# Optimization experiments

Hardware: AMD Instinct MI355X
Metric: run time of the kernel (lower is better)

Reference implementation:

```python
import jax, jax.numpy as jnp
import numpy as np

N_PATHOLOGY = 14      # NUM_PATHOLOGY_NODES (CheXpert/NIH pathology count)
NEG_SLOPE = 0.2       # PyG GATv2Conv default negative_slope


def gatv2_layer(x, src, dst, n_nodes, Wl, bl, Wr, br, att, bias, concat):
    """PyG GATv2Conv (share_weights=False, dropout inactive in eval).
    Wl/bl: source (lin_l) transform; Wr/br: target (lin_r) transform.
    att: [H, C] attention vector; bias: output bias.
    """
    H, C = att.shape
    xl = (x @ Wl + bl).reshape(-1, H, C)   # [N, H, C] source features
    xr = (x @ Wr + br).reshape(-1, H, C)   # [N, H, C] target features
    xj = xl[src]                            # [E, H, C] gathered source msgs
    xi = xr[dst]                            # [E, H, C] gathered targets
    s = jax.nn.leaky_relu(xi + xj, NEG_SLOPE)
    e = jnp.einsum('ehc,hc->eh', s, att)    # [E, H] raw attention logits
    # segment softmax over incoming edges of each destination node
    m = jax.ops.segment_max(e, dst, num_segments=n_nodes)      # [N, H]
    e = jnp.exp(e - m[dst])
    denom = jax.ops.segment_sum(e, dst, num_segments=n_nodes)  # [N, H]
    alpha = e / (denom[dst] + 1e-16)
    out = jax.ops.segment_sum(alpha[:, :, None] * xj, dst, num_segments=n_nodes)
    out = out.reshape(n_nodes, H * C) if concat else out.mean(axis=1)
    return out + bias


def setup_inputs() -> dict:
    key = jax.random.key(0)
    ks = jax.random.split(key, 16)
    N, E, D, H = 10000, 50000, 768, 4
    s = 0.02
    inp = {
        'x': jax.random.normal(ks[0], (N, D), jnp.float32),
        'edge_index': jax.random.randint(ks[1], (2, E), 0, N, jnp.int32),
        # layer 1: in=768 -> heads=4, out=768 (concat -> 3072)
        'Wl1': jax.random.normal(ks[2], (D, H * D), jnp.float32) * s,
        'bl1': jnp.zeros((H * D,), jnp.float32),
        'Wr1': jax.random.normal(ks[3], (D, H * D), jnp.float32) * s,
        'br1': jnp.zeros((H * D,), jnp.float32),
        'att1': jax.random.normal(ks[4], (H, D), jnp.float32) * s,
        'bias1': jnp.zeros((H * D,), jnp.float32),
        # layer 2: in=3072 -> heads=1, out=768 (mean/no-concat)
        'Wl2': jax.random.normal(ks[5], (H * D, D), jnp.float32) * s,
        'bl2': jnp.zeros((D,), jnp.float32),
        'Wr2': jax.random.normal(ks[6], (H * D, D), jnp.float32) * s,
        'br2': jnp.zeros((D,), jnp.float32),
        'att2': jax.random.normal(ks[7], (1, D), jnp.float32) * s,
        'bias2': jnp.zeros((D,), jnp.float32),
    }
    return inp


def reference(x, edge_index, Wl1, bl1, Wr1, br1, att1, bias1,
              Wl2, bl2, Wr2, br2, att2, bias2):
    n = x.shape[0]
    # PyG GATv2Conv adds self loops by default
    loops = jnp.arange(n, dtype=edge_index.dtype)
    src = jnp.concatenate([edge_index[0], loops])
    dst = jnp.concatenate([edge_index[1], loops])
    h = gatv2_layer(x, src, dst, n, Wl1, bl1, Wr1, br1, att1, bias1, True)
    h = jax.nn.relu(h)  # dropout is identity in eval mode
    out = gatv2_layer(h, src, dst, n, Wl2, bl2, Wr2, br2, att2, bias2, False)
    return out[:N_PATHOLOGY]
```

## Files before the change

kernel.cpp:

```cpp
#include <hip/hip_runtime.h>
#include <cstdint>
#include <cstddef>

#define N_PATH 14
#define NEG_SLOPE 0.2f
#define BINW 128
#define NZ2 4

using u16 = unsigned short;
using u32 = unsigned int;
typedef __attribute__((ext_vector_type(4))) float f32x4;
typedef __attribute__((ext_vector_type(8))) short bf16x8;

__device__ __forceinline__ float lrelu(float v) { return v > 0.f ? v : NEG_SLOPE * v; }
__device__ __forceinline__ u16 f2bf(float f) {
    union { float f; u32 u; } c; c.f = f;
    return (u16)((c.u + 0x7FFFu + ((c.u >> 16) & 1u)) >> 16);
}
__device__ __forceinline__ float bf2f(u16 v) {
    union { u32 u; float f; } c; c.u = ((u32)v) << 16; return c.f;
}

__global__ void k_init(int* __restrict__ mapBC, int nMap,
                       u32* __restrict__ z, int nZ)
{
    int stride = gridDim.x * blockDim.x;
    int i0 = blockIdx.x * blockDim.x + threadIdx.x;
    for (int i = i0; i < nMap; i += stride) mapBC[i] = -1;
    for (int i = i0; i < nZ; i += stride) z[i] = 0;
}

__global__ void k_build2(const int* __restrict__ esrc, const int* __restrict__ edst,
                         int E, int Nn,
                         int* __restrict__ mapB, int* __restrict__ listB,
                         int* __restrict__ cnt,
                         int* __restrict__ deg2, int* __restrict__ e2bin,
                         int capB)
{
    int e = blockIdx.x * blockDim.x + threadIdx.x;
    int ET = E + Nn;
    if (e >= ET) return;
    int s, d;
    if (e < E) { s = esrc[e]; d = edst[e]; } else { s = e - E; d = s; }
    if (d >= N_PATH) return;
    int slot = atomicAdd(&deg2[d], 1);
    if (slot < BINW) e2bin[d * BINW + slot] = s;
    int old = atomicCAS(&mapB[s], -1, -2);
    if (old == -1) {
        int idx = atomicAdd(&cnt[0], 1);
        if (idx < capB) listB[idx] = s;
        mapB[s] = idx;
    }
}

__global__ void k_build1(const int* __restrict__ esrc, const int* __restrict__ edst,
                         int E, int Nn,
                         const int* __restrict__ mapB,
                         int* __restrict__ mapC, int* __restrict__ listC,
                         int* __restrict__ cnt,
                         int* __restrict__ deg1, int* __restrict__ e1bin,
                         int capB, int capC)
{
    int e = blockIdx.x * blockDim.x + threadIdx.x;
    int ET = E + Nn;
    if (e >= ET) return;
    int s, d;
    if (e < E) { s = esrc[e]; d = edst[e]; } else { s = e - E; d = s; }
    int b = mapB[d];
    if (b < 0 || b >= capB) return;
    int slot = atomicAdd(&deg1[b], 1);
    if (slot < BINW) e1bin[b * BINW + slot] = s;
    int old = atomicCAS(&mapC[s], -1, -2);
    if (old == -1) {
        int idx = atomicAdd(&cnt[1], 1);
        if (idx < capC) listC[idx] = s;
        mapC[s] = idx;
    }
}

__global__ void k_gatherA(const float* __restrict__ x,
                          const int* __restrict__ listC, const int* __restrict__ listB,
                          const int* __restrict__ mapC, const int* __restrict__ cnt,
                          u16* __restrict__ Abf, int* __restrict__ listBinC,
                          int capB, int capC)
{
    int bid = blockIdx.x;
    int t = threadIdx.x;
    if (bid == capC) {
        int nB = cnt[0]; if (nB > capB) nB = capB;
        for (int i = t; i < capB; i += 192) {
            int v = 0;
            if (i < nB) {
                v = mapC[listB[i]];
                if (v < 0) v = 0;
                if (v >= capC) v = capC - 1;
            }
            listBinC[i] = v;
        }
        return;
    }
    int nC = cnt[1]; if (nC > capC) nC = capC;
    if (bid >= nC) return;
    int g = listC[bid];
    float4 v = *reinterpret_cast<const float4*>(x + (size_t)g * 768 + t * 4);
    uint2 o;
    o.x = (u32)f2bf(v.x) | ((u32)f2bf(v.y) << 16);
    o.y = (u32)f2bf(v.z) | ((u32)f2bf(v.w) << 16);
    *reinterpret_cast<uint2*>(Abf + (size_t)bid * 768 + t * 4) = o;
}

__device__ __forceinline__
void gemm_tile(const u16* __restrict__ A, int lda,
               const int* __restrict__ gather,
               const float* __restrict__ W, int ldw, int nColOff,
               const float* __restrict__ bias,
               void* __restrict__ Cout, int ldc, int mode,
               int M, int bx, int by, int k0, int kchunk,
               u16* __restrict__ As, u16* __restrict__ Bs)
{
    int m0 = by * 64;
    if (m0 >= M) return;
    int n0 = bx * 64;
    int t = threadIdx.x;
    int lane = t & 63, wave = t >> 6;
    int wr = wave >> 1, wc = wave & 1;
    int lrow = lane & 15, lhi = lane >> 4;

    int chunk = t & 7;
    int rowp[2], aRow[2], wIdx[2];
    #pragma unroll
    for (int p = 0; p < 2; ++p) {
        rowp[p] = p * 32 + (t >> 3);
        int ar = m0 + rowp[p]; if (ar >= M) ar = M - 1;
        aRow[p] = gather ? gather[ar] : ar;
        wIdx[p] = rowp[p] * 64 + ((chunk ^ (rowp[p] & 7)) << 3);
    }
    int bk = t >> 4;
    int bn = (t & 15) << 2;

    int aIdx[2][2], bIdx[2][2];
    #pragma unroll
    for (int mi = 0; mi < 2; ++mi)
        #pragma unroll
        for (int ks = 0; ks < 2; ++ks) {
            int ra = wr * 32 + mi * 16 + lrow;
            aIdx[mi][ks] = ra * 64 + ((((ks << 2) | lhi) ^ (ra & 7)) << 3);
            int rb = wc * 32 + mi * 16 + lrow;
            bIdx[mi][ks] = rb * 64 + ((((ks << 2) | lhi) ^ (rb & 7)) << 3);
        }

    f32x4 acc[2][2];
    #pragma unroll
    for (int i = 0; i < 2; ++i)
        #pragma unroll
        for (int j = 0; j < 2; ++j)
            acc[i][j] = (f32x4){0.f, 0.f, 0.f, 0.f};

    for (int kt = 0; kt < kchunk; kt += 64) {
        int kb = k0 + kt;
        #pragma unroll
        for (int p = 0; p < 2; ++p) {
            uint4 av = *reinterpret_cast<const uint4*>(
                A + (size_t)aRow[p] * lda + kb + chunk * 8);
            *reinterpret_cast<uint4*>(&As[wIdx[p]]) = av;
        }
        #pragma unroll
        for (int p = 0; p < 4; ++p) {
            int kk = p * 16 + bk;
            const float* wp = W + (size_t)(kb + kk) * ldw + nColOff + n0 + bn;
            float4 wv = *reinterpret_cast<const float4*>(wp);
            float wa[4] = {wv.x, wv.y, wv.z, wv.w};
            #pragma unroll
            for (int j = 0; j < 4; ++j) {
                int n = bn + j;
                int pc = (kk & 7) | ((((kk >> 3) & 7) ^ (n & 7)) << 3);
                Bs[n * 64 + pc] = f2bf(wa[j]);
            }
        }
        __syncthreads();
        #pragma unroll
        for (int ks = 0; ks < 2; ++ks) {
            bf16x8 a0 = *reinterpret_cast<const bf16x8*>(&As[aIdx[0][ks]]);
            bf16x8 a1 = *reinterpret_cast<const bf16x8*>(&As[aIdx[1][ks]]);
            bf16x8 b0 = *reinterpret_cast<const bf16x8*>(&Bs[bIdx[0][ks]]);
            bf16x8 b1 = *reinterpret_cast<const bf16x8*>(&Bs[bIdx[1][ks]]);
            acc[0][0] = __builtin_amdgcn_mfma_f32_16x16x32_bf16(a0, b0, acc[0][0], 0, 0, 0);
            acc[0][1] = __builtin_amdgcn_mfma_f32_16x16x32_bf16(a0, b1, acc[0][1], 0, 0, 0);
            acc[1][0] = __builtin_amdgcn_mfma_f32_16x16x32_bf16(a1, b0, acc[1][0], 0, 0, 0);
            acc[1][1] = __builtin_amdgcn_mfma_f32_16x16x32_bf16(a1, b1, acc[1][1], 0, 0, 0);
        }
        __syncthreads();
    }

    #pragma unroll
    for (int mi = 0; mi < 2; ++mi)
        #pragma unroll
        for (int ni = 0; ni < 2; ++ni) {
            int gc = n0 + wc * 32 + ni * 16 + lrow;
            float bv = (mode == 2) ? bias[gc] : 0.f;
            #pragma unroll
            for (int j = 0; j < 4; ++j) {
                int gr = m0 + wr * 32 + mi * 16 + lhi * 4 + j;
                if (gr < M) {
                    float v = acc[mi][ni][j] + bv;
                    if (mode == 2) ((u16*)Cout)[(size_t)gr * ldc + gc] = f2bf(v);
                    else           ((float*)Cout)[(size_t)gr * ldc + gc] = v;
                }
            }
        }
}

__global__ __launch_bounds__(256)
void k_gemm1(const u16* __restrict__ Abf, const int* __restrict__ listBinC,
             const float* __restrict__ Wl1, const float* __restrict__ Wr1,
             const float* __restrict__ bl1, const float* __restrict__ br1,
             u16* __restrict__ XL1, u16* __restrict__ XR1,
             const int* __restrict__ cnt, int capC, int capB)
{
    __shared__ __align__(16) u16 As[64 * 64];
    __shared__ __align__(16) u16 Bs[64 * 64];
    int partA = 48 * (capC / 64);
    int bid = blockIdx.x;
    if (bid < partA) {
        int nC = cnt[1]; if (nC > capC) nC = capC;
        gemm_tile(Abf, 768, nullptr, Wl1, 3072, 0, bl1, XL1, 3072, 2,
                  nC, bid % 48, bid / 48, 0, 768, As, Bs);
    } else {
        bid -= partA;
        int nB = cnt[0]; if (nB > capB) nB = capB;
        gemm_tile(Abf, 768, listBinC, Wr1, 3072, 0, br1, XR1, 3072, 2,
                  nB, bid % 48, bid / 48, 0, 768, As, Bs);
    }
}

__global__ __launch_bounds__(256)
void k_gemm2(const u16* __restrict__ H1bf,
             const float* __restrict__ Wl2, const float* __restrict__ Wr2,
             float* __restrict__ XLR2,
             const int* __restrict__ cnt, int capB)
{
    __shared__ __align__(16) u16 As[64 * 64];
    __shared__ __align__(16) u16 Bs[64 * 64];
    int nB = cnt[0]; if (nB > capB) nB = capB;
    int z = blockIdx.z;
    int n0 = blockIdx.x * 64;
    bool hi = n0 >= 768;
    const float* W = hi ? Wr2 : Wl2;
    int nColOff = hi ? -768 : 0;
    const int kchunk = 3072 / NZ2;
    float* Cp = XLR2 + (size_t)z * capB * 1536;
    gemm_tile(H1bf, 3072, nullptr, W, 768, nColOff, nullptr, Cp, 1536, 0,
              nB, blockIdx.x, blockIdx.y, z * kchunk, kchunk, As, Bs);
}

__global__ __launch_bounds__(256)
void k_fused1(const u16* __restrict__ XL1, const u16* __restrict__ XR1,
              const float* __restrict__ att1, const float* __restrict__ bias1,
              const int* __restrict__ mapC,
              const int* __restrict__ deg1, const int* __restrict__ e1bin,
              u16* __restrict__ H1bf,
              const int* __restrict__ cnt, int capB, int capC)
{
    __shared__ int sIdx[BINW];
    int b = blockIdx.x;
    int nB = cnt[0]; if (nB > capB) nB = capB;
    if (b >= nB) return;
    int t = threadIdx.x;
    int n = deg1[b]; if (n > BINW) n = BINW;
    if (t < n) {
        int c = mapC[e1bin[b * BINW + t]];
        if (c < 0) c = 0; if (c >= capC) c = capC - 1;
        sIdx[t] = c;
    }
    __syncthreads();

    int base = t * 12;
    float xr[12], av[12];
    {
        const u16* p = XR1 + (size_t)b * 3072 + base;
        uint2 q0 = *reinterpret_cast<const uint2*>(p);
        uint2 q1 = *reinterpret_cast<const uint2*>(p + 4);
        uint2 q2 = *reinterpret_cast<const uint2*>(p + 8);
        u32 w[6] = {q0.x, q0.y, q1.x, q1.y, q2.x, q2.y};
        #pragma unroll
        for (int j = 0; j < 6; ++j) {
            xr[2*j]   = bf2f((u16)(w[j] & 0xFFFF));
            xr[2*j+1] = bf2f((u16)(w[j] >> 16));
        }
        float4 a0 = *reinterpret_cast<const float4*>(att1 + base);
        float4 a1 = *reinterpret_cast<const float4*>(att1 + base + 4);
        float4 a2 = *reinterpret_cast<const float4*>(att1 + base + 8);
        av[0]=a0.x; av[1]=a0.y; av[2]=a0.z; av[3]=a0.w;
        av[4]=a1.x; av[5]=a1.y; av[6]=a1.z; av[7]=a1.w;
        av[8]=a2.x; av[9]=a2.y; av[10]=a2.z; av[11]=a2.w;
    }

    float acc[12];
    #pragma unroll
    for (int j = 0; j < 12; ++j) acc[j] = 0.f;
    float sumex = 0.f;

    uint2 q0, q1, q2;
    if (n > 0) {
        const u16* p = XL1 + (size_t)sIdx[0] * 3072 + base;
        q0 = *reinterpret_cast<const uint2*>(p);
        q1 = *reinterpret_cast<const uint2*>(p + 4);
        q2 = *reinterpret_cast<const uint2*>(p + 8);
    }
    for (int i = 0; i < n; ++i) {
        uint2 r0 = q0, r1 = q1, r2 = q2;
        if (i + 1 < n) {
            const u16* p = XL1 + (size_t)sIdx[i + 1] * 3072 + base;
            q0 = *reinterpret_cast<const uint2*>(p);
            q1 = *reinterpret_cast<const uint2*>(p + 4);
            q2 = *reinterpret_cast<const uint2*>(p + 8);
        }
        float xl[12];
        u32 w[6] = {r0.x, r0.y, r1.x, r1.y, r2.x, r2.y};
        #pragma unroll
        for (int j = 0; j < 6; ++j) {
            xl[2*j]   = bf2f((u16)(w[j] & 0xFFFF));
            xl[2*j+1] = bf2f((u16)(w[j] >> 16));
        }
        float pa = 0.f;
        #pragma unroll
        for (int j = 0; j < 12; ++j)
            pa = fmaf(av[j], lrelu(xl[j] + xr[j]), pa);
        #pragma unroll
        for (int off = 32; off > 0; off >>= 1) pa += __shfl_xor(pa, off);
        float ex = expf(pa);
        sumex += ex;
        #pragma unroll
        for (int j = 0; j < 12; ++j) acc[j] = fmaf(ex, xl[j], acc[j]);
    }

    float inv = 1.f / (sumex + 1e-16f);
    u32 o[6];
    #pragma unroll
    for (int j = 0; j < 6; ++j) {
        float v0 = acc[2*j]   * inv + bias1[base + 2*j];
        float v1 = acc[2*j+1] * inv + bias1[base + 2*j+1];
        v0 = v0 > 0.f ? v0 : 0.f;
        v1 = v1 > 0.f ? v1 : 0.f;
        o[j] = (u32)f2bf(v0) | ((u32)f2bf(v1) << 16);
    }
    u16* q = H1bf + (size_t)b * 3072 + base;
    uint2 s0; s0.x = o[0]; s0.y = o[1];
    uint2 s1; s1.x = o[2]; s1.y = o[3];
    uint2 s2; s2.x = o[4]; s2.y = o[5];
    *reinterpret_cast<uint2*>(q)     = s0;
    *reinterpret_cast<uint2*>(q + 4) = s1;
    *reinterpret_cast<uint2*>(q + 8) = s2;
}

__global__ __launch_bounds__(256)
void k_fused2(const float* __restrict__ XLR2,
              const float* __restrict__ att2, const float* __restrict__ bias2,
              const float* __restrict__ bl2, const float* __restrict__ br2,
              const int* __restrict__ mapB,
              const int* __restrict__ deg2, const int* __restrict__ e2bin,
              float* __restrict__ out, int capB)
{
    __shared__ int sIdx[BINW];
    __shared__ float sAcc[4][768];
    __shared__ float sSum[4];
    const size_t PART = (size_t)capB * 1536;
    int a = blockIdx.x;
    int t = threadIdx.x;
    int wv = t >> 6, lane = t & 63;
    int n = deg2[a]; if (n > BINW) n = BINW;
    if (t < n) {
        int bs = mapB[e2bin[a * BINW + t]];
        if (bs < 0) bs = 0; if (bs >= capB) bs = capB - 1;
        sIdx[t] = bs;
    }
    __syncthreads();

    int base = lane * 12;
    int bd = mapB[a];
    if (bd < 0) bd = 0; if (bd >= capB) bd = capB - 1;

    float xr[12], av[12], blv[12];
    {
        const float* p = XLR2 + (size_t)bd * 1536 + 768 + base;
        #pragma unroll
        for (int j = 0; j < 12; ++j) xr[j] = br2[base + j];
        for (int z = 0; z < NZ2; ++z)
            #pragma unroll
            for (int j = 0; j < 12; ++j) xr[j] += p[z * PART + j];
        #pragma unroll
        for (int j = 0; j < 12; ++j) { av[j] = att2[base + j]; blv[j] = bl2[base + j]; }
    }

    float acc[12];
    #pragma unroll
    for (int j = 0; j < 12; ++j) acc[j] = 0.f;
    float sumex = 0.f;

    for (int i = wv; i < n; i += 4) {
        int bs = sIdx[i];
        const float* p = XLR2 + (size_t)bs * 1536 + base;
        float xl[12];
        #pragma unroll
        for (int j = 0; j < 12; ++j) xl[j] = blv[j];
        for (int z = 0; z < NZ2; ++z)
            #pragma unroll
            for (int j = 0; j < 12; ++j) xl[j] += p[z * PART + j];
        float pa = 0.f;
        #pragma unroll
        for (int j = 0; j < 12; ++j)
            pa = fmaf(av[j], lrelu(xl[j] + xr[j]), pa);
        #pragma unroll
        for (int off = 32; off > 0; off >>= 1) pa += __shfl_xor(pa, off);
        float ex = expf(pa);
        sumex += ex;
        #pragma unroll
        for (int j = 0; j < 12; ++j) acc[j] = fmaf(ex, xl[j], acc[j]);
    }

    if (lane == 0) sSum[wv] = sumex;
    #pragma unroll
    for (int j = 0; j < 12; ++j) sAcc[wv][base + j] = acc[j];
    __syncthreads();

    float tot = sSum[0] + sSum[1] + sSum[2] + sSum[3];
    float inv = 1.f / (tot + 1e-16f);
    for (int c = t; c < 768; c += 256) {
        float s = sAcc[0][c] + sAcc[1][c] + sAcc[2][c] + sAcc[3][c];
        out[(size_t)a * 768 + c] = s * inv + bias2[c];
    }
}

struct Lay {
    size_t mapB, mapC;
    size_t zbase, zbytes;
    size_t cnt, deg2, deg1;
    size_t listB, listC, listBinC, e1bin, e2bin;
    size_t Abf, XL1, XR1, H1bf, XLR2;
    size_t total;
};

static Lay makeLayout(int Nn, int cB, int cC)
{
    Lay L{};
    size_t off = 0;
    auto take = [&](size_t bytes) { size_t o = (off + 255) & ~(size_t)255; off = o + bytes; return o; };
    L.mapB = take((size_t)2 * Nn * 4);
    L.mapC = L.mapB + (size_t)Nn * 4;
    size_t zo = 0;
    size_t cntO  = zo; zo += 64;
    size_t deg2O = zo; zo += 64 * 4;
    size_t deg1O = zo; zo += (size_t)cB * 4;
    L.zbase = take(zo); L.zbytes = zo;
    L.cnt  = L.zbase + cntO;
    L.deg2 = L.zbase + deg2O;
    L.deg1 = L.zbase + deg1O;
    L.listB    = take((size_t)cB * 4);
    L.listC    = take((size_t)cC * 4);
    L.listBinC = take((size_t)cB * 4);
    L.e1bin = take((size_t)cB * BINW * 4);
    L.e2bin = take((size_t)16 * BINW * 4);
    L.Abf  = take((size_t)cC * 768 * 2);
    L.XL1  = take((size_t)cC * 3072 * 2);
    L.XR1  = take((size_t)cB * 3072 * 2);
    L.H1bf = take((size_t)cB * 3072 * 2);
    L.XLR2 = take((size_t)NZ2 * cB * 1536 * 4);
    L.total = off;
    return L;
}

extern "C" void kernel_launch(void* const* d_in, const int* in_sizes, int n_in,
                              void* d_out, int out_size, void* d_ws, size_t ws_size,
                              hipStream_t stream)
{
    const float* x     = (const float*)d_in[0];
    const int*   ei    = (const int*)  d_in[1];
    const float* Wl1   = (const float*)d_in[2];
    const float* bl1   = (const float*)d_in[3];
    const float* Wr1   = (const float*)d_in[4];
    const float* br1   = (const float*)d_in[5];
    const float* att1  = (const float*)d_in[6];
    const float* bias1 = (const float*)d_in[7];
    const float* Wl2   = (const float*)d_in[8];
    const float* bl2   = (const float*)d_in[9];
    const float* Wr2   = (const float*)d_in[10];
    const float* br2   = (const float*)d_in[11];
    const float* att2  = (const float*)d_in[12];
    const float* bias2 = (const float*)d_in[13];
    float* out = (float*)d_out;

    int Nn = in_sizes[0] / 768;
    int E  = in_sizes[1] / 2;
    const int* esrc = ei;
    const int* edst = ei + E;
    int ET = E + Nn;

    static const int tiers[2][2] = { {256, 1024}, {128, 768} };
    int capB = tiers[1][0], capC = tiers[1][1];
    Lay L = makeLayout(Nn, capB, capC);
    for (int t = 0; t < 2; ++t) {
        Lay cand = makeLayout(Nn, tiers[t][0], tiers[t][1]);
        if (cand.total <= ws_size) { capB = tiers[t][0]; capC = tiers[t][1]; L = cand; break; }
    }

    char* ws = (char*)d_ws;
    int*   mapB     = (int*)  (ws + L.mapB);
    int*   mapC     = (int*)  (ws + L.mapC);
    int*   cnt      = (int*)  (ws + L.cnt);
    int*   deg2     = (int*)  (ws + L.deg2);
    int*   deg1     = (int*)  (ws + L.deg1);
    int*   listB    = (int*)  (ws + L.listB);
    int*   listC    = (int*)  (ws + L.listC);
    int*   listBinC = (int*)  (ws + L.listBinC);
    int*   e1bin    = (int*)  (ws + L.e1bin);
    int*   e2bin    = (int*)  (ws + L.e2bin);
    u16*   Abf      = (u16*)  (ws + L.Abf);
    u16*   XL1      = (u16*)  (ws + L.XL1);
    u16*   XR1      = (u16*)  (ws + L.XR1);
    u16*   H1bf     = (u16*)  (ws + L.H1bf);
    float* XLR2     = (float*)(ws + L.XLR2);

    k_init<<<256, 256, 0, stream>>>((int*)(ws + L.mapB), 2 * Nn,
                                    (u32*)(ws + L.zbase), (int)(L.zbytes / 4));

    int bgrid = (ET + 255) / 256;
    k_build2<<<bgrid, 256, 0, stream>>>(esrc, edst, E, Nn, mapB, listB, cnt,
                                        deg2, e2bin, capB);
    k_build1<<<bgrid, 256, 0, stream>>>(esrc, edst, E, Nn, mapB, mapC, listC, cnt,
                                        deg1, e1bin, capB, capC);

    k_gatherA<<<capC + 1, 192, 0, stream>>>(x, listC, listB, mapC, cnt,
                                            Abf, listBinC, capB, capC);

    int g1 = 48 * (capC / 64) + 48 * (capB / 64);
    k_gemm1<<<g1, 256, 0, stream>>>(Abf, listBinC, Wl1, Wr1, bl1, br1,
                                    XL1, XR1, cnt, capC, capB);

    k_fused1<<<capB, 256, 0, stream>>>(XL1, XR1, att1, bias1, mapC, deg1, e1bin,
                                       H1bf, cnt, capB, capC);

    k_gemm2<<<dim3(24, capB / 64, NZ2), 256, 0, stream>>>(H1bf, Wl2, Wr2, XLR2,
                                                          cnt, capB);

    k_fused2<<<N_PATH, 256, 0, stream>>>(XLR2, att2, bias2, bl2, br2, mapB,
                                         deg2, e2bin, out, capB);
}
```

Measured before the change: 87.54 us.

## Fuse all stages into one persistent kernel with software grid barriers

Replaces the seven separate launches (two graph builds, gather, two GEMMs, two fused attention stages) with one persistent 512-block kernel. The stages are separated by an atomic-counter grid barrier, and the kernel sizes its GEMM tile loops from the actual node counts. The aim is to remove per-launch overhead and the tail gaps between small kernels. In exchange it relies on all 512 blocks being co-resident (otherwise the barrier deadlocks), adds barrier latency, and puts the small stages on idle or oversubscribed blocks.

```diff
diff --git a/kernel.cpp b/kernel.cpp
--- a/kernel.cpp
+++ b/kernel.cpp
@@ -6,6 +6,7 @@
 #define NEG_SLOPE 0.2f
 #define BINW 128
 #define NZ2 4
+#define NBLK 512
 
 using u16 = unsigned short;
 using u32 = unsigned int;
@@ -20,6 +21,42 @@
 __device__ __forceinline__ float bf2f(u16 v) {
     union { u32 u; float f; } c; c.u = ((u32)v) << 16; return c.f;
 }
+__device__ __forceinline__ int imin(int a, int b) { return a < b ? a : b; }
+
+struct Params {
+    const float* x; const int* esrc; const int* edst;
+    const float *Wl1, *bl1, *Wr1, *br1, *att1, *bias1;
+    const float *Wl2, *bl2, *Wr2, *br2, *att2, *bias2;
+    float* out;
+    int *mapB, *mapC, *cnt; unsigned* bar; int *deg2, *deg1;
+    int *listB, *listC, *listBinC, *e1bin, *e2bin;
+    u16 *Abf, *XL1, *XR1, *H1bf; float* XLR2;
+    int Nn, E, capB, capC;
+};
+
+__device__ __forceinline__ void gridbar(unsigned* bar, unsigned& mygen)
+{
+    __syncthreads();
+    if (threadIdx.x == 0) {
+        __threadfence();
+        unsigned nblk = gridDim.x;
+        unsigned prev = atomicAdd(&bar[0], 1u);
+        if (prev == nblk - 1u) {
+            atomicExch(&bar[0], 0u);
+            __threadfence();
+            atomicAdd(&bar[1], 1u);
+        } else {
+            unsigned g;
+            do {
+                __builtin_amdgcn_s_sleep(4);
+                g = __hip_atomic_load(&bar[1], __ATOMIC_RELAXED, __HIP_MEMORY_SCOPE_AGENT);
+            } while (g == mygen);
+        }
+        mygen++;
+        __threadfence();
+    }
+    __syncthreads();
+}
 
 __global__ void k_init(int* __restrict__ mapBC, int nMap,
                        u32* __restrict__ z, int nZ)
@@ -28,85 +65,6 @@
     int i0 = blockIdx.x * blockDim.x + threadIdx.x;
     for (int i = i0; i < nMap; i += stride) mapBC[i] = -1;
     for (int i = i0; i < nZ; i += stride) z[i] = 0;
-}
-
-__global__ void k_build2(const int* __restrict__ esrc, const int* __restrict__ edst,
-                         int E, int Nn,
-                         int* __restrict__ mapB, int* __restrict__ listB,
-                         int* __restrict__ cnt,
-                         int* __restrict__ deg2, int* __restrict__ e2bin,
-                         int capB)
-{
-    int e = blockIdx.x * blockDim.x + threadIdx.x;
-    int ET = E + Nn;
-    if (e >= ET) return;
-    int s, d;
-    if (e < E) { s = esrc[e]; d = edst[e]; } else { s = e - E; d = s; }
-    if (d >= N_PATH) return;
-    int slot = atomicAdd(&deg2[d], 1);
-    if (slot < BINW) e2bin[d * BINW + slot] = s;
-    int old = atomicCAS(&mapB[s], -1, -2);
-    if (old == -1) {
-        int idx = atomicAdd(&cnt[0], 1);
-        if (idx < capB) listB[idx] = s;
-        mapB[s] = idx;
-    }
-}
-
-__global__ void k_build1(const int* __restrict__ esrc, const int* __restrict__ edst,
-                         int E, int Nn,
-                         const int* __restrict__ mapB,
-                         int* __restrict__ mapC, int* __restrict__ listC,
-                         int* __restrict__ cnt,
-                         int* __restrict__ deg1, int* __restrict__ e1bin,
-                         int capB, int capC)
-{
-    int e = blockIdx.x * blockDim.x + threadIdx.x;
-    int ET = E + Nn;
-    if (e >= ET) return;
-    int s, d;
-    if (e < E) { s = esrc[e]; d = edst[e]; } else { s = e - E; d = s; }
-    int b = mapB[d];
-    if (b < 0 || b >= capB) return;
-    int slot = atomicAdd(&deg1[b], 1);
-    if (slot < BINW) e1bin[b * BINW + slot] = s;
-    int old = atomicCAS(&mapC[s], -1, -2);
-    if (old == -1) {
-        int idx = atomicAdd(&cnt[1], 1);
-        if (idx < capC) listC[idx] = s;
-        mapC[s] = idx;
-    }
-}
-
-__global__ void k_gatherA(const float* __restrict__ x,
-                          const int* __restrict__ listC, const int* __restrict__ listB,
-                          const int* __restrict__ mapC, const int* __restrict__ cnt,
-                          u16* __restrict__ Abf, int* __restrict__ listBinC,
-                          int capB, int capC)
-{
-    int bid = blockIdx.x;
-    int t = threadIdx.x;
-    if (bid == capC) {
-        int nB = cnt[0]; if (nB > capB) nB = capB;
-        for (int i = t; i < capB; i += 192) {
-            int v = 0;
-            if (i < nB) {
-                v = mapC[listB[i]];
-                if (v < 0) v = 0;
-                if (v >= capC) v = capC - 1;
-            }
-            listBinC[i] = v;
-        }
-        return;
-    }
-    int nC = cnt[1]; if (nC > capC) nC = capC;
-    if (bid >= nC) return;
-    int g = listC[bid];
-    float4 v = *reinterpret_cast<const float4*>(x + (size_t)g * 768 + t * 4);
-    uint2 o;
-    o.x = (u32)f2bf(v.x) | ((u32)f2bf(v.y) << 16);
-    o.y = (u32)f2bf(v.z) | ((u32)f2bf(v.w) << 16);
-    *reinterpret_cast<uint2*>(Abf + (size_t)bid * 768 + t * 4) = o;
 }
 
 __device__ __forceinline__
@@ -129,11 +87,11 @@
     int chunk = t & 7;
     int rowp[2], aRow[2], wIdx[2];
     #pragma unroll
-    for (int p = 0; p < 2; ++p) {
-        rowp[p] = p * 32 + (t >> 3);
-        int ar = m0 + rowp[p]; if (ar >= M) ar = M - 1;
-        aRow[p] = gather ? gather[ar] : ar;
-        wIdx[p] = rowp[p] * 64 + ((chunk ^ (rowp[p] & 7)) << 3);
+    for (int pp = 0; pp < 2; ++pp) {
+        rowp[pp] = pp * 32 + (t >> 3);
+        int ar = m0 + rowp[pp]; if (ar >= M) ar = M - 1;
+        aRow[pp] = gather ? gather[ar] : ar;
+        wIdx[pp] = rowp[pp] * 64 + ((chunk ^ (rowp[pp] & 7)) << 3);
     }
     int bk = t >> 4;
     int bn = (t & 15) << 2;
@@ -159,14 +117,14 @@
     for (int kt = 0; kt < kchunk; kt += 64) {
         int kb = k0 + kt;
         #pragma unroll
-        for (int p = 0; p < 2; ++p) {
+        for (int pp = 0; pp < 2; ++pp) {
             uint4 av = *reinterpret_cast<const uint4*>(
-                A + (size_t)aRow[p] * lda + kb + chunk * 8);
-            *reinterpret_cast<uint4*>(&As[wIdx[p]]) = av;
-        }
-        #pragma unroll
-        for (int p = 0; p < 4; ++p) {
-            int kk = p * 16 + bk;
+                A + (size_t)aRow[pp] * lda + kb + chunk * 8);
+            *reinterpret_cast<uint4*>(&As[wIdx[pp]]) = av;
+        }
+        #pragma unroll
+        for (int pp = 0; pp < 4; ++pp) {
+            int kk = pp * 16 + bk;
             const float* wp = W + (size_t)(kb + kk) * ldw + nColOff + n0 + bn;
             float4 wv = *reinterpret_cast<const float4*>(wp);
             float wa[4] = {wv.x, wv.y, wv.z, wv.w};
@@ -210,66 +168,14 @@
         }
 }
 
-__global__ __launch_bounds__(256)
-void k_gemm1(const u16* __restrict__ Abf, const int* __restrict__ listBinC,
-             const float* __restrict__ Wl1, const float* __restrict__ Wr1,
-             const float* __restrict__ bl1, const float* __restrict__ br1,
-             u16* __restrict__ XL1, u16* __restrict__ XR1,
-             const int* __restrict__ cnt, int capC, int capB)
-{
-    __shared__ __align__(16) u16 As[64 * 64];
-    __shared__ __align__(16) u16 Bs[64 * 64];
-    int partA = 48 * (capC / 64);
-    int bid = blockIdx.x;
-    if (bid < partA) {
-        int nC = cnt[1]; if (nC > capC) nC = capC;
-        gemm_tile(Abf, 768, nullptr, Wl1, 3072, 0, bl1, XL1, 3072, 2,
-                  nC, bid % 48, bid / 48, 0, 768, As, Bs);
-    } else {
-        bid -= partA;
-        int nB = cnt[0]; if (nB > capB) nB = capB;
-        gemm_tile(Abf, 768, listBinC, Wr1, 3072, 0, br1, XR1, 3072, 2,
-                  nB, bid % 48, bid / 48, 0, 768, As, Bs);
-    }
-}
-
-__global__ __launch_bounds__(256)
-void k_gemm2(const u16* __restrict__ H1bf,
-             const float* __restrict__ Wl2, const float* __restrict__ Wr2,
-             float* __restrict__ XLR2,
-             const int* __restrict__ cnt, int capB)
-{
-    __shared__ __align__(16) u16 As[64 * 64];
-    __shared__ __align__(16) u16 Bs[64 * 64];
-    int nB = cnt[0]; if (nB > capB) nB = capB;
-    int z = blockIdx.z;
-    int n0 = blockIdx.x * 64;
-    bool hi = n0 >= 768;
-    const float* W = hi ? Wr2 : Wl2;
-    int nColOff = hi ? -768 : 0;
-    const int kchunk = 3072 / NZ2;
-    float* Cp = XLR2 + (size_t)z * capB * 1536;
-    gemm_tile(H1bf, 3072, nullptr, W, 768, nColOff, nullptr, Cp, 1536, 0,
-              nB, blockIdx.x, blockIdx.y, z * kchunk, kchunk, As, Bs);
-}
-
-__global__ __launch_bounds__(256)
-void k_fused1(const u16* __restrict__ XL1, const u16* __restrict__ XR1,
-              const float* __restrict__ att1, const float* __restrict__ bias1,
-              const int* __restrict__ mapC,
-              const int* __restrict__ deg1, const int* __restrict__ e1bin,
-              u16* __restrict__ H1bf,
-              const int* __restrict__ cnt, int capB, int capC)
-{
-    __shared__ int sIdx[BINW];
-    int b = blockIdx.x;
-    int nB = cnt[0]; if (nB > capB) nB = capB;
-    if (b >= nB) return;
+__device__ __forceinline__
+void fused1_body(const Params& P, int b, int* sIdx)
+{
     int t = threadIdx.x;
-    int n = deg1[b]; if (n > BINW) n = BINW;
+    int n = P.deg1[b]; if (n > BINW) n = BINW;
     if (t < n) {
-        int c = mapC[e1bin[b * BINW + t]];
-        if (c < 0) c = 0; if (c >= capC) c = capC - 1;
+        int c = P.mapC[P.e1bin[b * BINW + t]];
+        if (c < 0) c = 0; if (c >= P.capC) c = P.capC - 1;
         sIdx[t] = c;
     }
     __syncthreads();
@@ -277,19 +183,19 @@
     int base = t * 12;
     float xr[12], av[12];
     {
-        const u16* p = XR1 + (size_t)b * 3072 + base;
-        uint2 q0 = *reinterpret_cast<const uint2*>(p);
-        uint2 q1 = *reinterpret_cast<const uint2*>(p + 4);
-        uint2 q2 = *reinterpret_cast<const uint2*>(p + 8);
+        const u16* q = P.XR1 + (size_t)b * 3072 + base;
+        uint2 q0 = *reinterpret_cast<const uint2*>(q);
+        uint2 q1 = *reinterpret_cast<const uint2*>(q + 4);
+        uint2 q2 = *reinterpret_cast<const uint2*>(q + 8);
         u32 w[6] = {q0.x, q0.y, q1.x, q1.y, q2.x, q2.y};
         #pragma unroll
         for (int j = 0; j < 6; ++j) {
             xr[2*j]   = bf2f((u16)(w[j] & 0xFFFF));
             xr[2*j+1] = bf2f((u16)(w[j] >> 16));
         }
-        float4 a0 = *reinterpret_cast<const float4*>(att1 + base);
-        float4 a1 = *reinterpret_cast<const float4*>(att1 + base + 4);
-        float4 a2 = *reinterpret_cast<const float4*>(att1 + base + 8);
+        float4 a0 = *reinterpret_cast<const float4*>(P.att1 + base);
+        float4 a1 = *reinterpret_cast<const float4*>(P.att1 + base + 4);
+        float4 a2 = *reinterpret_cast<const float4*>(P.att1 + base + 8);
         av[0]=a0.x; av[1]=a0.y; av[2]=a0.z; av[3]=a0.w;
         av[4]=a1.x; av[5]=a1.y; av[6]=a1.z; av[7]=a1.w;
         av[8]=a2.x; av[9]=a2.y; av[10]=a2.z; av[11]=a2.w;
@@ -302,18 +208,18 @@
 
     uint2 q0, q1, q2;
     if (n > 0) {
-        const u16* p = XL1 + (size_t)sIdx[0] * 3072 + base;
-        q0 = *reinterpret_cast<const uint2*>(p);
-        q1 = *reinterpret_cast<const uint2*>(p + 4);
-        q2 = *reinterpret_cast<const uint2*>(p + 8);
+        const u16* q = P.XL1 + (size_t)sIdx[0] * 3072 + base;
+        q0 = *reinterpret_cast<const uint2*>(q);
+        q1 = *reinterpret_cast<const uint2*>(q + 4);
+        q2 = *reinterpret_cast<const uint2*>(q + 8);
     }
     for (int i = 0; i < n; ++i) {
         uint2 r0 = q0, r1 = q1, r2 = q2;
         if (i + 1 < n) {
-            const u16* p = XL1 + (size_t)sIdx[i + 1] * 3072 + base;
-            q0 = *reinterpret_cast<const uint2*>(p);
-            q1 = *reinterpret_cast<const uint2*>(p + 4);
-            q2 = *reinterpret_cast<const uint2*>(p + 8);
+            const u16* q = P.XL1 + (size_t)sIdx[i + 1] * 3072 + base;
+            q0 = *reinterpret_cast<const uint2*>(q);
+            q1 = *reinterpret_cast<const uint2*>(q + 4);
+            q2 = *reinterpret_cast<const uint2*>(q + 8);
         }
         float xl[12];
         u32 w[6] = {r0.x, r0.y, r1.x, r1.y, r2.x, r2.y};
@@ -338,13 +244,13 @@
     u32 o[6];
     #pragma unroll
     for (int j = 0; j < 6; ++j) {
-        float v0 = acc[2*j]   * inv + bias1[base + 2*j];
-        float v1 = acc[2*j+1] * inv + bias1[base + 2*j+1];
+        float v0 = acc[2*j]   * inv + P.bias1[base + 2*j];
+        float v1 = acc[2*j+1] * inv + P.bias1[base + 2*j+1];
         v0 = v0 > 0.f ? v0 : 0.f;
         v1 = v1 > 0.f ? v1 : 0.f;
         o[j] = (u32)f2bf(v0) | ((u32)f2bf(v1) << 16);
     }
-    u16* q = H1bf + (size_t)b * 3072 + base;
+    u16* q = P.H1bf + (size_t)b * 3072 + base;
     uint2 s0; s0.x = o[0]; s0.y = o[1];
     uint2 s1; s1.x = o[2]; s1.y = o[3];
     uint2 s2; s2.x = o[4]; s2.y = o[5];
@@ -353,43 +259,38 @@
     *reinterpret_cast<uint2*>(q + 8) = s2;
 }
 
-__global__ __launch_bounds__(256)
-void k_fused2(const float* __restrict__ XLR2,
-              const float* __restrict__ att2, const float* __restrict__ bias2,
-              const float* __restrict__ bl2, const float* __restrict__ br2,
-              const int* __restrict__ mapB,
-              const int* __restrict__ deg2, const int* __restrict__ e2bin,
-              float* __restrict__ out, int capB)
-{
-    __shared__ int sIdx[BINW];
-    __shared__ float sAcc[4][768];
-    __shared__ float sSum[4];
-    const size_t PART = (size_t)capB * 1536;
-    int a = blockIdx.x;
+__device__ __forceinline__
+void fused2_body(const Params& P, int a, char* smem)
+{
+    int* sIdx = (int*)smem;
+    float (*sAcc)[768] = (float (*)[768])(smem + 512);
+    float* sSum = (float*)(smem + 512 + 4 * 768 * 4);
+    const size_t PART = (size_t)P.capB * 1536;
+
     int t = threadIdx.x;
     int wv = t >> 6, lane = t & 63;
-    int n = deg2[a]; if (n > BINW) n = BINW;
+    int n = P.deg2[a]; if (n > BINW) n = BINW;
     if (t < n) {
-        int bs = mapB[e2bin[a * BINW + t]];
-        if (bs < 0) bs = 0; if (bs >= capB) bs = capB - 1;
+        int bs = P.mapB[P.e2bin[a * BINW + t]];
+        if (bs < 0) bs = 0; if (bs >= P.capB) bs = P.capB - 1;
         sIdx[t] = bs;
     }
     __syncthreads();
 
     int base = lane * 12;
-    int bd = mapB[a];
-    if (bd < 0) bd = 0; if (bd >= capB) bd = capB - 1;
+    int bd = P.mapB[a];
+    if (bd < 0) bd = 0; if (bd >= P.capB) bd = P.capB - 1;
 
     float xr[12], av[12], blv[12];
     {
-        const float* p = XLR2 + (size_t)bd * 1536 + 768 + base;
-        #pragma unroll
-        for (int j = 0; j < 12; ++j) xr[j] = br2[base + j];
+        const float* q = P.XLR2 + (size_t)bd * 1536 + 768 + base;
+        #pragma unroll
+        for (int j = 0; j < 12; ++j) xr[j] = P.br2[base + j];
         for (int z = 0; z < NZ2; ++z)
             #pragma unroll
-            for (int j = 0; j < 12; ++j) xr[j] += p[z * PART + j];
-        #pragma unroll
-        for (int j = 0; j < 12; ++j) { av[j] = att2[base + j]; blv[j] = bl2[base + j]; }
+            for (int j = 0; j < 12; ++j) xr[j] += q[z * PART + j];
+        #pragma unroll
+        for (int j = 0; j < 12; ++j) { av[j] = P.att2[base + j]; blv[j] = P.bl2[base + j]; }
     }
 
     float acc[12];
@@ -399,13 +300,13 @@
 
     for (int i = wv; i < n; i += 4) {
         int bs = sIdx[i];
-        const float* p = XLR2 + (size_t)bs * 1536 + base;
+        const float* q = P.XLR2 + (size_t)bs * 1536 + base;
         float xl[12];
         #pragma unroll
         for (int j = 0; j < 12; ++j) xl[j] = blv[j];
         for (int z = 0; z < NZ2; ++z)
             #pragma unroll
-            for (int j = 0; j < 12; ++j) xl[j] += p[z * PART + j];
+            for (int j = 0; j < 12; ++j) xl[j] += q[z * PART + j];
         float pa = 0.f;
         #pragma unroll
         for (int j = 0; j < 12; ++j)
@@ -427,14 +328,128 @@
     float inv = 1.f / (tot + 1e-16f);
     for (int c = t; c < 768; c += 256) {
         float s = sAcc[0][c] + sAcc[1][c] + sAcc[2][c] + sAcc[3][c];
-        out[(size_t)a * 768 + c] = s * inv + bias2[c];
+        P.out[(size_t)a * 768 + c] = s * inv + P.bias2[c];
+    }
+}
+
+__global__ __launch_bounds__(256, 2)
+void mega(Params P)
+{
+    __shared__ __align__(16) char smem[16384];
+    unsigned mygen = 0;
+    int gtid = blockIdx.x * blockDim.x + threadIdx.x;
+    int gstride = gridDim.x * blockDim.x;
+    int ET = P.E + P.Nn;
+
+    for (int e = gtid; e < ET; e += gstride) {
+        int s, d;
+        if (e < P.E) { s = P.esrc[e]; d = P.edst[e]; } else { s = e - P.E; d = s; }
+        if (d >= N_PATH) continue;
+        int slot = atomicAdd(&P.deg2[d], 1);
+        if (slot < BINW) P.e2bin[d * BINW + slot] = s;
+        int old = atomicCAS(&P.mapB[s], -1, -2);
+        if (old == -1) {
+            int idx = atomicAdd(&P.cnt[0], 1);
+            if (idx < P.capB) P.listB[idx] = s;
+            P.mapB[s] = idx;
+        }
+    }
+    gridbar(P.bar, mygen);
+
+    for (int e = gtid; e < ET; e += gstride) {
+        int s, d;
+        if (e < P.E) { s = P.esrc[e]; d = P.edst[e]; } else { s = e - P.E; d = s; }
+        int b = P.mapB[d];
+        if (b < 0 || b >= P.capB) continue;
+        int slot = atomicAdd(&P.deg1[b], 1);
+        if (slot < BINW) P.e1bin[b * BINW + slot] = s;
+        int old = atomicCAS(&P.mapC[s], -1, -2);
+        if (old == -1) {
+            int idx = atomicAdd(&P.cnt[1], 1);
+            if (idx < P.capC) P.listC[idx] = s;
+            P.mapC[s] = idx;
+        }
+    }
+    gridbar(P.bar, mygen);
+
+    int nB = imin(P.cnt[0], P.capB);
+    int nC = imin(P.cnt[1], P.capC);
+    for (int idx = gtid; idx < nC * 192; idx += gstride) {
+        int row = idx / 192;
+        int col = (idx - row * 192) * 4;
+        int g = P.listC[row];
+        float4 v = *reinterpret_cast<const float4*>(P.x + (size_t)g * 768 + col);
+        uint2 o;
+        o.x = (u32)f2bf(v.x) | ((u32)f2bf(v.y) << 16);
+        o.y = (u32)f2bf(v.z) | ((u32)f2bf(v.w) << 16);
+        *reinterpret_cast<uint2*>(P.Abf + (size_t)row * 768 + col) = o;
+    }
+    for (int i = gtid; i < P.capB; i += gstride) {
+        int v = 0;
+        if (i < nB) {
+            v = P.mapC[P.listB[i]];
+            if (v < 0) v = 0;
+            if (v >= P.capC) v = P.capC - 1;
+        }
+        P.listBinC[i] = v;
+    }
+    gridbar(P.bar, mygen);
+
+    {
+        u16* As = (u16*)smem;
+        u16* Bs = (u16*)(smem + 8192);
+        int rtC = (nC + 63) >> 6, rtB = (nB + 63) >> 6;
+        int tilesL = 48 * rtC, tilesR = 48 * rtB;
+        for (int tt = blockIdx.x; tt < tilesL + tilesR; tt += gridDim.x) {
+            if (tt < tilesL)
+                gemm_tile(P.Abf, 768, nullptr, P.Wl1, 3072, 0, P.bl1,
+                          P.XL1, 3072, 2, nC, tt % 48, tt / 48, 0, 768, As, Bs);
+            else {
+                int u = tt - tilesL;
+                gemm_tile(P.Abf, 768, P.listBinC, P.Wr1, 3072, 0, P.br1,
+                          P.XR1, 3072, 2, nB, u % 48, u / 48, 0, 768, As, Bs);
+            }
+        }
+    }
+    gridbar(P.bar, mygen);
+
+    for (int b = blockIdx.x; b < nB; b += gridDim.x) {
+        fused1_body(P, b, (int*)smem);
+        __syncthreads();
+    }
+    gridbar(P.bar, mygen);
+
+    {
+        u16* As = (u16*)smem;
+        u16* Bs = (u16*)(smem + 8192);
+        int rtB = (nB + 63) >> 6;
+        int ntiles = 24 * rtB * NZ2;
+        const int kchunk = 3072 / NZ2;
+        for (int tt = blockIdx.x; tt < ntiles; tt += gridDim.x) {
+            int bx = tt % 24;
+            int rest = tt / 24;
+            int by = rest % rtB;
+            int z = rest / rtB;
+            bool hi = bx >= 12;
+            const float* W = hi ? P.Wr2 : P.Wl2;
+            int nColOff = hi ? -768 : 0;
+            float* Cp = P.XLR2 + (size_t)z * P.capB * 1536;
+            gemm_tile(P.H1bf, 3072, nullptr, W, 768, nColOff, nullptr,
+                      Cp, 1536, 0, nB, bx, by, z * kchunk, kchunk, As, Bs);
+        }
+    }
+    gridbar(P.bar, mygen);
+
+    for (int a = blockIdx.x; a < N_PATH; a += gridDim.x) {
+        fused2_body(P, a, smem);
+        __syncthreads();
     }
 }
 
 struct Lay {
     size_t mapB, mapC;
     size_t zbase, zbytes;
-    size_t cnt, deg2, deg1;
+    size_t cnt, bar, deg2, deg1;
     size_t listB, listC, listBinC, e1bin, e2bin;
     size_t Abf, XL1, XR1, H1bf, XLR2;
     size_t total;
@@ -449,10 +464,12 @@
     L.mapC = L.mapB + (size_t)Nn * 4;
     size_t zo = 0;
     size_t cntO  = zo; zo += 64;
+    size_t barO  = zo; zo += 64;
     size_t deg2O = zo; zo += 64 * 4;
     size_t deg1O = zo; zo += (size_t)cB * 4;
     L.zbase = take(zo); L.zbytes = zo;
     L.cnt  = L.zbase + cntO;
+    L.bar  = L.zbase + barO;
     L.deg2 = L.zbase + deg2O;
     L.deg1 = L.zbase + deg1O;
     L.listB    = take((size_t)cB * 4);
@@ -475,25 +492,9 @@
 {
     const float* x     = (const float*)d_in[0];
     const int*   ei    = (const int*)  d_in[1];
-    const float* Wl1   = (const float*)d_in[2];
-    const float* bl1   = (const float*)d_in[3];
-    const float* Wr1   = (const float*)d_in[4];
-    const float* br1   = (const float*)d_in[5];
-    const float* att1  = (const float*)d_in[6];
-    const float* bias1 = (const float*)d_in[7];
-    const float* Wl2   = (const float*)d_in[8];
-    const float* bl2   = (const float*)d_in[9];
-    const float* Wr2   = (const float*)d_in[10];
-    const float* br2   = (const float*)d_in[11];
-    const float* att2  = (const float*)d_in[12];
-    const float* bias2 = (const float*)d_in[13];
-    float* out = (float*)d_out;
 
     int Nn = in_sizes[0] / 768;
     int E  = in_sizes[1] / 2;
-    const int* esrc = ei;
-    const int* edst = ei + E;
-    int ET = E + Nn;
 
     static const int tiers[2][2] = { {256, 1024}, {128, 768} };
     int capB = tiers[1][0], capC = tiers[1][1];
@@ -504,44 +505,44 @@
     }
 
     char* ws = (char*)d_ws;
-    int*   mapB     = (int*)  (ws + L.mapB);
-    int*   mapC     = (int*)  (ws + L.mapC);
-    int*   cnt      = (int*)  (ws + L.cnt);
-    int*   deg2     = (int*)  (ws + L.deg2);
-    int*   deg1     = (int*)  (ws + L.deg1);
-    int*   listB    = (int*)  (ws + L.listB);
-    int*   listC    = (int*)  (ws + L.listC);
-    int*   listBinC = (int*)  (ws + L.listBinC);
-    int*   e1bin    = (int*)  (ws + L.e1bin);
-    int*   e2bin    = (int*)  (ws + L.e2bin);
-    u16*   Abf      = (u16*)  (ws + L.Abf);
-    u16*   XL1      = (u16*)  (ws + L.XL1);
-    u16*   XR1      = (u16*)  (ws + L.XR1);
-    u16*   H1bf     = (u16*)  (ws + L.H1bf);
-    float* XLR2     = (float*)(ws + L.XLR2);
 
     k_init<<<256, 256, 0, stream>>>((int*)(ws + L.mapB), 2 * Nn,
                                     (u32*)(ws + L.zbase), (int)(L.zbytes / 4));
 
-    int bgrid = (ET + 255) / 256;
-    k_build2<<<bgrid, 256, 0, stream>>>(esrc, edst, E, Nn, mapB, listB, cnt,
-                                        deg2, e2bin, capB);
-    k_build1<<<bgrid, 256, 0, stream>>>(esrc, edst, E, Nn, mapB, mapC, listC, cnt,
-                                        deg1, e1bin, capB, capC);
-
-    k_gatherA<<<capC + 1, 192, 0, stream>>>(x, listC, listB, mapC, cnt,
-                                            Abf, listBinC, capB, capC);
-
-    int g1 = 48 * (capC / 64) + 48 * (capB / 64);
-    k_gemm1<<<g1, 256, 0, stream>>>(Abf, listBinC, Wl1, Wr1, bl1, br1,
-                                    XL1, XR1, cnt, capC, capB);
-
-    k_fused1<<<capB, 256, 0, stream>>>(XL1, XR1, att1, bias1, mapC, deg1, e1bin,
-                                       H1bf, cnt, capB, capC);
-
-    k_gemm2<<<dim3(24, capB / 64, NZ2), 256, 0, stream>>>(H1bf, Wl2, Wr2, XLR2,
-                                                          cnt, capB);
-
-    k_fused2<<<N_PATH, 256, 0, stream>>>(XLR2, att2, bias2, bl2, br2, mapB,
-                                         deg2, e2bin, out, capB);
-}
+    Params P;
+    P.x = x;
+    P.esrc = ei;
+    P.edst = ei + E;
+    P.Wl1   = (const float*)d_in[2];
+    P.bl1   = (const float*)d_in[3];
+    P.Wr1   = (const float*)d_in[4];
+    P.br1   = (const float*)d_in[5];
+    P.att1  = (const float*)d_in[6];
+    P.bias1 = (const float*)d_in[7];
+    P.Wl2   = (const float*)d_in[8];
+    P.bl2   = (const float*)d_in[9];
+    P.Wr2   = (const float*)d_in[10];
+    P.br2   = (const float*)d_in[11];
+    P.att2  = (const float*)d_in[12];
+    P.bias2 = (const float*)d_in[13];
+    P.out   = (float*)d_out;
+    P.mapB  = (int*)(ws + L.mapB);
+    P.mapC  = (int*)(ws + L.mapC);
+    P.cnt   = (int*)(ws + L.cnt);
+    P.bar   = (unsigned*)(ws + L.bar);
+    P.deg2  = (int*)(ws + L.deg2);
+    P.deg1  = (int*)(ws + L.deg1);
+    P.listB    = (int*)(ws + L.listB);
+    P.listC    = (int*)(ws + L.listC);
+    P.listBinC = (int*)(ws + L.listBinC);
+    P.e1bin = (int*)(ws + L.e1bin);
+    P.e2bin = (int*)(ws + L.e2bin);
+    P.Abf  = (u16*)(ws + L.Abf);
+    P.XL1  = (u16*)(ws + L.XL1);
+    P.XR1  = (u16*)(ws + L.XR1);
+    P.H1bf = (u16*)(ws + L.H1bf);
+    P.XLR2 = (float*)(ws + L.XLR2);
+    P.Nn = Nn; P.E = E; P.capB = capB; P.capC = capC;
+
+    mega<<<NBLK, 256, 0, stream>>>(P);
+}
```

Result: slower. 330.6 us (+277.6%).
